# Optimization experiments

Measured on AMD Instinct MI355X. Metric: run time of the kernel, lower is better.

## Reference

```python
import jax, jax.numpy as jnp
import numpy as np

B, T, T3, P = 512, 128, 64, 12
IN1, H1 = 64, 256
IN2, H2 = 64, 256
IN3, H3 = 32, 128
GLOB, OUT = 32, 2
FC_IN = 2 * H1 + H2 + GLOB + 2 * P * H3  # 3872


def lstm_last(x, Wih, Whh, bih, bhh):
    """Single-layer batch-first LSTM (PyTorch gate order i,f,g,o); returns last hidden state [B,H]."""
    Bx = x.shape[0]
    H = Whh.shape[1]
    # precompute input projections for all timesteps: [T, B, 4H]
    xg = jnp.swapaxes(jnp.einsum('bti,gi->btg', x, Wih) + bih + bhh, 0, 1)

    def step(carry, g):
        h, c = carry
        gates = g + h @ Whh.T
        i, f, gg, o = jnp.split(gates, 4, axis=-1)
        c = jax.nn.sigmoid(f) * c + jax.nn.sigmoid(i) * jnp.tanh(gg)
        h = jax.nn.sigmoid(o) * jnp.tanh(c)
        return (h, c), None

    h0 = jnp.zeros((Bx, H), x.dtype)
    (h, _), _ = jax.lax.scan(step, (h0, h0), xg)
    return h


def setup_inputs() -> dict:
    key = jax.random.key(0)
    ks = jax.random.split(key, 20)
    n = lambda k, s: jax.random.normal(k, s, dtype=jnp.float32)
    w = lambda k, s: jax.random.normal(k, s, dtype=jnp.float32) * 0.05
    return {
        'current_game': n(ks[0], (B, GLOB)),
        'games_home': n(ks[1], (B, T, IN1)),
        'games_away': n(ks[2], (B, T, IN1)),
        'games_vs': n(ks[3], (B, T, IN2)),
        'players_home': n(ks[4], (B, P, T3, IN3)),
        'players_away': n(ks[5], (B, P, T3, IN3)),
        'Wih1': w(ks[6], (4 * H1, IN1)), 'Whh1': w(ks[7], (4 * H1, H1)),
        'bih1': w(ks[8], (4 * H1,)), 'bhh1': w(ks[9], (4 * H1,)),
        'Wih2': w(ks[10], (4 * H2, IN2)), 'Whh2': w(ks[11], (4 * H2, H2)),
        'bih2': w(ks[12], (4 * H2,)), 'bhh2': w(ks[13], (4 * H2,)),
        'Wih3': w(ks[14], (4 * H3, IN3)), 'Whh3': w(ks[15], (4 * H3, H3)),
        'bih3': w(ks[16], (4 * H3,)), 'bhh3': w(ks[17], (4 * H3,)),
        'Wfc': w(ks[18], (OUT, FC_IN)), 'bfc': w(ks[19], (OUT,)),
    }


def reference(current_game, games_home, games_away, games_vs, players_home, players_away,
              Wih1, Whh1, bih1, bhh1, Wih2, Whh2, bih2, bhh2, Wih3, Whh3, bih3, bhh3,
              Wfc, bfc):
    h_home = lstm_last(games_home, Wih1, Whh1, bih1, bhh1)   # [B, H1]
    h_away = lstm_last(games_away, Wih1, Whh1, bih1, bhh1)   # shared rnn weights
    h_vs = lstm_last(games_vs, Wih2, Whh2, bih2, bhh2)       # [B, H2]

    def players_feat(xp):
        # fold the player dim into batch: one batched LSTM pass instead of P launches
        b, p = xp.shape[0], xp.shape[1]
        h = lstm_last(xp.reshape(b * p, xp.shape[2], xp.shape[3]), Wih3, Whh3, bih3, bhh3)
        return h.reshape(b, p * H3)  # concat in player order, matching the torch loop

    feat = jnp.concatenate([
        h_home, h_away, h_vs,
        players_feat(players_home), players_feat(players_away),
        current_game,
    ], axis=1)  # [B, FC_IN]
    return feat @ Wfc.T + bfc
```

## Files before the change

### kernel.cpp

```cpp
#include <hip/hip_runtime.h>
#include <stdint.h>

typedef __bf16 bf16;
typedef bf16 bf16x8 __attribute__((ext_vector_type(8)));
typedef bf16 bf16x4 __attribute__((ext_vector_type(4)));
typedef float f32x4 __attribute__((ext_vector_type(4)));
typedef int i32x4 __attribute__((ext_vector_type(4)));

#define DEV __device__ __forceinline__

static const size_t OFF_W1 = 0;
static const size_t OFF_W2 = OFF_W1 + (size_t)640 * 1024;
static const size_t OFF_W3 = OFF_W2 + (size_t)640 * 1024;
static const size_t OFF_B1 = OFF_W3 + (size_t)160 * 1024;
static const size_t OFF_B2 = OFF_B1 + 4096;
static const size_t OFF_B3 = OFF_B2 + 4096;
static const size_t OFF_FEAT = OFF_B3 + 2048;
static const size_t WS_NEEDED = OFF_FEAT + (size_t)512 * 3840 * 4;

DEV float sigm(float x) { return 1.f / (1.f + __expf(-x)); }
DEV float tanh_(float x) { return 1.f - 2.f / (__expf(2.f * x) + 1.f); }

DEV void mfma_bv(f32x4& acc, i32x4 a, i32x4 b) {
  asm("v_mfma_f32_16x16x32_bf16 %0, %1, %2, %0" : "+a"(acc) : "v"(a), "v"(b));
}
DEV void mfma_ba(f32x4& acc, i32x4 a, i32x4 b) {
  asm("v_mfma_f32_16x16x32_bf16 %0, %1, %2, %0" : "+a"(acc) : "v"(a), "a"(b));
}

template <int H, int IN, int NT, int NKT>
DEV void packW(const float* __restrict__ Wih, const float* __restrict__ Whh,
               bf16* __restrict__ dst, int i) {
  int e = i & 7, lane = (i >> 3) & 63;
  int rest = i >> 9;
  int kt = rest % NKT; rest /= NKT;
  int nt = rest % NT;  int w = rest / NT;
  int quad = lane >> 4, l16 = lane & 15;
  constexpr int NTG = NT / 4, UW = NT * 4;
  int unit = w * UW + (nt % NTG) * 16 + l16;
  int g = nt / NTG;
  int r = g * H + unit;
  int k = kt * 32 + quad * 8 + e;
  float v = (k < IN) ? Wih[r * IN + k] : Whh[r * H + (k - IN)];
  dst[i] = (bf16)v;
}

__global__ void prep_kernel(const float* __restrict__ Wih1, const float* __restrict__ Whh1,
                            const float* __restrict__ bih1, const float* __restrict__ bhh1,
                            const float* __restrict__ Wih2, const float* __restrict__ Whh2,
                            const float* __restrict__ bih2, const float* __restrict__ bhh2,
                            const float* __restrict__ Wih3, const float* __restrict__ Whh3,
                            const float* __restrict__ bih3, const float* __restrict__ bhh3,
                            uint8_t* __restrict__ ws) {
  const int gt = blockIdx.x * blockDim.x + threadIdx.x;
  const int gs = gridDim.x * blockDim.x;
  bf16* W1 = (bf16*)(ws + OFF_W1);
  bf16* W2 = (bf16*)(ws + OFF_W2);
  bf16* W3 = (bf16*)(ws + OFF_W3);
  float* B1 = (float*)(ws + OFF_B1);
  float* B2 = (float*)(ws + OFF_B2);
  float* B3 = (float*)(ws + OFF_B3);
  for (int i = gt; i < 640 * 512; i += gs) {
    packW<256, 64, 16, 10>(Wih1, Whh1, W1, i);
    packW<256, 64, 16, 10>(Wih2, Whh2, W2, i);
  }
  for (int i = gt; i < 160 * 512; i += gs) packW<128, 32, 8, 5>(Wih3, Whh3, W3, i);
  for (int i = gt; i < 1024; i += gs) { B1[i] = bih1[i] + bhh1[i]; B2[i] = bih2[i] + bhh2[i]; }
  for (int i = gt; i < 512; i += gs) B3[i] = bih3[i] + bhh3[i];
}

template <int BM, int IN, int H, int T, int NT, int NKT, int NVV, int NVA, int NL, int NS,
          int DOM>
DEV void lstm_tile3(const float* __restrict__ x0, const float* __restrict__ x1, int halfM,
                    const bf16* __restrict__ Wd, const float* __restrict__ bsum,
                    float* __restrict__ feat, int mg, uint8_t* smem) {
  static_assert(NVV + NVA + NL + NS == NT, "split");
  static_assert((NL == 0 && NS == 0) || (NKT % 2 == 0), "wrap parity");
  constexpr int MT = BM / 16;
  constexpr int NTG = NT / 4;
  constexpr int UW = NT * 4;
  constexpr int KCH = (IN + H) / 8;
  constexpr int SROW = KCH + 1;
  constexpr int AROWE = SROW * 8;
  constexpr int XPT = BM * IN / 4 / 256;

  const int tid = threadIdx.x;
  const int lane = tid & 63;
  const int w = tid >> 6;
  const int quad = lane >> 4;
  const int l16 = lane & 15;
  const int rowbase = mg * BM;

  bf16* A = (bf16*)smem;
  bf16* Wshm = (bf16*)(smem + (size_t)BM * AROWE * 2);

  const float* xb = (rowbase < halfM) ? x0 : x1;
  const int rowoff = rowbase - ((rowbase < halfM) ? 0 : halfM);

  {
    constexpr int HCH = KCH - IN / 8;
    for (int i = tid; i < BM * HCH * 4; i += 256) {
      int row = i / (HCH * 4), rem = i % (HCH * 4);
      int chunk = IN / 8 + rem / 4, d = rem % 4;
      ((uint32_t*)A)[row * SROW * 4 + chunk * 4 + d] = 0;
    }
  }
  if constexpr (NL > 0) {
    for (int idx = tid; idx < 4 * NL * NKT * 64; idx += 256) {
      int ln = idx & 63;
      int kt = (idx >> 6) % NKT;
      int rest = (idx >> 6) / NKT;
      int nl = rest % NL, w2 = rest / NL;
      int blob = (w2 * NT + NVV + NVA + nl) * NKT + kt;
      *(bf16x8*)(Wshm + (size_t)((w2 * NL + nl) * NKT + kt) * 512 + ln * 8) =
          *(const bf16x8*)(Wd + (size_t)blob * 512 + ln * 8);
    }
  }
  i32x4 wregv[NVV > 0 ? NVV : 1][NKT];
  {
    const bf16* Wv = Wd + (size_t)(w * NT) * NKT * 512 + lane * 8;
#pragma unroll
    for (int nt = 0; nt < NVV; ++nt)
#pragma unroll
      for (int kt = 0; kt < NKT; ++kt)
        wregv[nt][kt] = *(const i32x4*)(Wv + (size_t)(nt * NKT + kt) * 512);
  }
  i32x4 wrega[NVA > 0 ? NVA : 1][NKT];
  {
    const bf16* Wa = Wd + (size_t)(w * NT + NVV) * NKT * 512 + lane * 8;
#pragma unroll
    for (int nt = 0; nt < NVA; ++nt)
#pragma unroll
      for (int kt = 0; kt < NKT; ++kt)
        wrega[nt][kt] = *(const i32x4*)(Wa + (size_t)(nt * NKT + kt) * 512);
  }
  const bf16* Wstream = Wd + (size_t)(w * NT + NVV + NVA + NL) * NKT * 512 + lane * 8;

  float bias[4][NTG];
#pragma unroll
  for (int g = 0; g < 4; ++g)
#pragma unroll
    for (int ut = 0; ut < NTG; ++ut)
      bias[g][ut] = bsum[g * H + w * UW + ut * 16 + l16];

  i32x4 sbuf[2][NS > 0 ? NS : 1];
  i32x4 wlds[2][NL > 0 ? NL : 1];

  float4 xr[XPT];
#pragma unroll
  for (int i = 0; i < XPT; ++i) {
    int idx = i * 256 + tid;
    int row = idx / (IN / 4), c4 = idx % (IN / 4);
    xr[i] = *(const float4*)(xb + (size_t)(rowoff + row) * T * IN + c4 * 4);
  }
#pragma unroll
  for (int i = 0; i < XPT; ++i) {
    int idx = i * 256 + tid;
    int row = idx / (IN / 4), c4 = idx % (IN / 4);
    int k = c4 * 4;
    bf16x4 p;
    p[0] = (bf16)xr[i].x; p[1] = (bf16)xr[i].y; p[2] = (bf16)xr[i].z; p[3] = (bf16)xr[i].w;
    *(bf16x4*)(A + row * AROWE + (k >> 3) * 8 + (k & 7)) = p;
  }
  __syncthreads();
  if constexpr (NS > 0) {
#pragma unroll
    for (int ns = 0; ns < NS; ++ns)
      sbuf[0][ns] = *(const i32x4*)(Wstream + (size_t)(ns * NKT) * 512);
  }
  if constexpr (NL > 0) {
#pragma unroll
    for (int nl = 0; nl < NL; ++nl)
      wlds[0][nl] = *(const i32x4*)(Wshm + (size_t)((w * NL + nl) * NKT) * 512 + lane * 8);
  }

  float c[MT * NTG * 4];
#pragma unroll
  for (int i = 0; i < MT * NTG * 4; ++i) c[i] = 0.f;

  f32x4 acc[NT][MT];
#pragma unroll
  for (int nt = 0; nt < NT; ++nt)
#pragma unroll
    for (int mt = 0; mt < MT; ++mt) acc[nt][mt] = f32x4{0.f, 0.f, 0.f, 0.f};

  i32x4 afbuf[2][MT];

#pragma unroll 1
  for (int t = 0; t < T; ++t) {
#pragma unroll
    for (int mt = 0; mt < MT; ++mt)
      afbuf[0][mt] = *(const i32x4*)(A + (mt * 16 + l16) * AROWE + quad * 8);
    if (t < T - 1) {
#pragma unroll
      for (int i = 0; i < XPT; ++i) {
        int idx = i * 256 + tid;
        int row = idx / (IN / 4), c4 = idx % (IN / 4);
        xr[i] =
            *(const float4*)(xb + (size_t)(rowoff + row) * T * IN + (size_t)(t + 1) * IN + c4 * 4);
      }
    }
#pragma unroll
    for (int kt = 0; kt < NKT; ++kt) {
      const int ktn = (kt + 1) % NKT;
      const int pc = kt & 1, pn = (kt + 1) & 1;
      if (kt + 1 < NKT) {
#pragma unroll
        for (int mt = 0; mt < MT; ++mt)
          afbuf[pn][mt] = *(const i32x4*)(A + (mt * 16 + l16) * AROWE + ((kt + 1) * 4 + quad) * 8);
      }
      if constexpr (NS > 0) {
#pragma unroll
        for (int ns = 0; ns < NS; ++ns)
          sbuf[pn][ns] = *(const i32x4*)(Wstream + (size_t)(ns * NKT + ktn) * 512);
      }
      if constexpr (NL > 0) {
#pragma unroll
        for (int nl = 0; nl < NL; ++nl)
          wlds[pn][nl] = *(const i32x4*)(Wshm + (size_t)((w * NL + nl) * NKT + ktn) * 512 + lane * 8);
      }
#pragma unroll
      for (int nt = 0; nt < NVV; ++nt)
#pragma unroll
        for (int mt = 0; mt < MT; ++mt) mfma_bv(acc[nt][mt], afbuf[pc][mt], wregv[nt][kt]);
#pragma unroll
      for (int nt = 0; nt < NVA; ++nt)
#pragma unroll
        for (int mt = 0; mt < MT; ++mt) mfma_ba(acc[NVV + nt][mt], afbuf[pc][mt], wrega[nt][kt]);
      if constexpr (NL > 0) {
#pragma unroll
        for (int nl = 0; nl < NL; ++nl)
#pragma unroll
          for (int mt = 0; mt < MT; ++mt)
            mfma_bv(acc[NVV + NVA + nl][mt], afbuf[pc][mt], wlds[pc][nl]);
      }
      if constexpr (NS > 0) {
#pragma unroll
        for (int ns = 0; ns < NS; ++ns)
#pragma unroll
          for (int mt = 0; mt < MT; ++mt)
            mfma_bv(acc[NVV + NVA + NL + ns][mt], afbuf[pc][mt], sbuf[pc][ns]);
      }
    }
    __syncthreads();
    asm volatile("s_nop 7\n\ts_nop 7\n\ts_nop 7" ::);

#pragma unroll
    for (int mt = 0; mt < MT; ++mt)
#pragma unroll
      for (int ut = 0; ut < NTG; ++ut)
#pragma unroll
        for (int j = 0; j < 4; ++j) {
          float gi = acc[0 * NTG + ut][mt][j] + bias[0][ut];
          float gf = acc[1 * NTG + ut][mt][j] + bias[1][ut];
          float gg = acc[2 * NTG + ut][mt][j] + bias[2][ut];
          float go = acc[3 * NTG + ut][mt][j] + bias[3][ut];
          int ci = (mt * NTG + ut) * 4 + j;
          float cc = sigm(gf) * c[ci] + sigm(gi) * tanh_(gg);
          c[ci] = cc;
          float hv = sigm(go) * tanh_(cc);
          int row = mt * 16 + quad * 4 + j;
          if (t < T - 1) {
            int k = IN + w * UW + ut * 16 + l16;
            A[row * AROWE + (k >> 3) * 8 + (k & 7)] = (bf16)hv;
          } else {
            int R = rowbase + row;
            int unit = w * UW + ut * 16 + l16;
            int b, col;
            if (DOM == 0) {
              if (R < 512) { b = R; col = unit; }
              else         { b = R - 512; col = 256 + unit; }
            } else if (DOM == 1) {
              b = R; col = 512 + unit;
            } else {
              int rr = R; int base = 768;
              if (rr >= 6144) { rr -= 6144; base = 2304; }
              b = rr / 12; int p = rr - b * 12;
              col = base + p * 128 + unit;
            }
            feat[(size_t)b * 3840 + col] = hv;
          }
        }
#pragma unroll
    for (int nt = 0; nt < NT; ++nt)
#pragma unroll
      for (int mt = 0; mt < MT; ++mt) acc[nt][mt] = f32x4{0.f, 0.f, 0.f, 0.f};
    if (t < T - 1) {
#pragma unroll
      for (int i = 0; i < XPT; ++i) {
        int idx = i * 256 + tid;
        int row = idx / (IN / 4), c4 = idx % (IN / 4);
        int k = c4 * 4;
        bf16x4 p;
        p[0] = (bf16)xr[i].x; p[1] = (bf16)xr[i].y; p[2] = (bf16)xr[i].z; p[3] = (bf16)xr[i].w;
        *(bf16x4*)(A + row * AROWE + (k >> 3) * 8 + (k & 7)) = p;
      }
    }
    __syncthreads();
  }
}

template <int NL1, int NS1>
DEV void lstm_body(const float* gh, const float* ga, const float* gv, const float* ph,
                   const float* pa, uint8_t* ws, uint8_t* smem) {
  float* feat = (float*)(ws + OFF_FEAT);
  int bid = blockIdx.x;
  if (bid < 64) {
    lstm_tile3<16, 64, 256, 128, 16, 10, 2, 4, NL1, NS1, 0>(
        gh, ga, 512, (const bf16*)(ws + OFF_W1), (const float*)(ws + OFF_B1), feat, bid, smem);
  } else if (bid < 96) {
    lstm_tile3<16, 64, 256, 128, 16, 10, 2, 4, NL1, NS1, 1>(
        gv, gv, 512, (const bf16*)(ws + OFF_W2), (const float*)(ws + OFF_B2), feat, bid - 64, smem);
  } else {
    lstm_tile3<32, 32, 128, 64, 8, 5, 8, 0, 0, 0, 2>(
        ph, pa, 6144, (const bf16*)(ws + OFF_W3), (const float*)(ws + OFF_B3), feat, bid - 96, smem);
  }
}

__global__ __launch_bounds__(256, 1) void lstm_main_big(const float* __restrict__ gh,
                                                        const float* __restrict__ ga,
                                                        const float* __restrict__ gv,
                                                        const float* __restrict__ ph,
                                                        const float* __restrict__ pa,
                                                        uint8_t* __restrict__ ws) {
  extern __shared__ uint8_t smem[];
  lstm_body<2, 8>(gh, ga, gv, ph, pa, ws, smem);
}

__global__ __launch_bounds__(256, 1) void lstm_main_small(const float* __restrict__ gh,
                                                          const float* __restrict__ ga,
                                                          const float* __restrict__ gv,
                                                          const float* __restrict__ ph,
                                                          const float* __restrict__ pa,
                                                          uint8_t* __restrict__ ws) {
  extern __shared__ uint8_t smem[];
  lstm_body<1, 9>(gh, ga, gv, ph, pa, ws, smem);
}

__global__ void fc_kernel(const float* __restrict__ feat, const float* __restrict__ cg,
                          const float* __restrict__ Wfc, const float* __restrict__ bfc,
                          float* __restrict__ out) {
  int b = blockIdx.x, tid = threadIdx.x;
  float a0 = 0.f, a1 = 0.f;
  for (int c = tid; c < 3840; c += 256) {
    float f = feat[(size_t)b * 3840 + c];
    a0 += f * Wfc[c];
    a1 += f * Wfc[3872 + c];
  }
  if (tid < 32) {
    float f = cg[b * 32 + tid];
    a0 += f * Wfc[3840 + tid];
    a1 += f * Wfc[3872 + 3840 + tid];
  }
#pragma unroll
  for (int o = 32; o > 0; o >>= 1) {
    a0 += __shfl_down(a0, o);
    a1 += __shfl_down(a1, o);
  }
  __shared__ float red[8];
  int wv = tid >> 6;
  if ((tid & 63) == 0) { red[wv * 2] = a0; red[wv * 2 + 1] = a1; }
  __syncthreads();
  if (tid == 0) {
    out[b * 2 + 0] = red[0] + red[2] + red[4] + red[6] + bfc[0];
    out[b * 2 + 1] = red[1] + red[3] + red[5] + red[7] + bfc[1];
  }
}

extern "C" void kernel_launch(void* const* d_in, const int* in_sizes, int n_in, void* d_out,
                              int out_size, void* d_ws, size_t ws_size, hipStream_t stream) {
  const float* cg = (const float*)d_in[0];
  const float* gh = (const float*)d_in[1];
  const float* ga = (const float*)d_in[2];
  const float* gv = (const float*)d_in[3];
  const float* ph = (const float*)d_in[4];
  const float* pa = (const float*)d_in[5];
  const float* Wih1 = (const float*)d_in[6];
  const float* Whh1 = (const float*)d_in[7];
  const float* bih1 = (const float*)d_in[8];
  const float* bhh1 = (const float*)d_in[9];
  const float* Wih2 = (const float*)d_in[10];
  const float* Whh2 = (const float*)d_in[11];
  const float* bih2 = (const float*)d_in[12];
  const float* bhh2 = (const float*)d_in[13];
  const float* Wih3 = (const float*)d_in[14];
  const float* Whh3 = (const float*)d_in[15];
  const float* bih3 = (const float*)d_in[16];
  const float* bhh3 = (const float*)d_in[17];
  const float* Wfc = (const float*)d_in[18];
  const float* bfc = (const float*)d_in[19];
  uint8_t* ws = (uint8_t*)d_ws;
  if (ws_size < WS_NEEDED) return;

  hipLaunchKernelGGL(prep_kernel, dim3(512), dim3(256), 0, stream, Wih1, Whh1, bih1, bhh1,
                     Wih2, Whh2, bih2, bhh2, Wih3, Whh3, bih3, bhh3, ws);

  int dev = 0, maxShm = 0;
  (void)hipGetDevice(&dev);
  (void)hipDeviceGetAttribute(&maxShm, hipDeviceAttributeMaxSharedMemoryPerBlock, dev);
  hipError_t ae = hipFuncSetAttribute((const void*)lstm_main_big,
                                      hipFuncAttributeMaxDynamicSharedMemorySize, 92416);
  if (ae == hipSuccess && maxShm >= 92416) {
    hipLaunchKernelGGL(lstm_main_big, dim3(480), dim3(256), 92416, stream, gh, ga, gv, ph, pa, ws);
  } else {
    hipLaunchKernelGGL(lstm_main_small, dim3(480), dim3(256), 51456, stream, gh, ga, gv, ph, pa,
                       ws);
  }
  hipLaunchKernelGGL(fc_kernel, dim3(512), dim3(256), 0, stream,
                     (const float*)(ws + OFF_FEAT), cg, Wfc, bfc, (float*)d_out);
}
```

Before: 1.899 ms.

## Split activations into bf16 hi/lo halves and run LSTM tiles with eight waves

```diff
diff --git a/kernel.cpp b/kernel.cpp
--- a/kernel.cpp
+++ b/kernel.cpp
@@ -24,9 +24,6 @@
 DEV void mfma_bv(f32x4& acc, i32x4 a, i32x4 b) {
   asm("v_mfma_f32_16x16x32_bf16 %0, %1, %2, %0" : "+a"(acc) : "v"(a), "v"(b));
 }
-DEV void mfma_ba(f32x4& acc, i32x4 a, i32x4 b) {
-  asm("v_mfma_f32_16x16x32_bf16 %0, %1, %2, %0" : "+a"(acc) : "v"(a), "a"(b));
-}
 
 template <int H, int IN, int NT, int NKT>
 DEV void packW(const float* __restrict__ Wih, const float* __restrict__ Whh,
@@ -36,7 +33,7 @@
   int kt = rest % NKT; rest /= NKT;
   int nt = rest % NT;  int w = rest / NT;
   int quad = lane >> 4, l16 = lane & 15;
-  constexpr int NTG = NT / 4, UW = NT * 4;
+  constexpr int NTG = NT / 4 > 0 ? NT / 4 : 1, UW = NT * 4;
   int unit = w * UW + (nt % NTG) * 16 + l16;
   int g = nt / NTG;
   int r = g * H + unit;
@@ -61,28 +58,29 @@
   float* B2 = (float*)(ws + OFF_B2);
   float* B3 = (float*)(ws + OFF_B3);
   for (int i = gt; i < 640 * 512; i += gs) {
-    packW<256, 64, 16, 10>(Wih1, Whh1, W1, i);
-    packW<256, 64, 16, 10>(Wih2, Whh2, W2, i);
-  }
-  for (int i = gt; i < 160 * 512; i += gs) packW<128, 32, 8, 5>(Wih3, Whh3, W3, i);
+    packW<256, 64, 8, 10>(Wih1, Whh1, W1, i);
+    packW<256, 64, 8, 10>(Wih2, Whh2, W2, i);
+  }
+  for (int i = gt; i < 160 * 512; i += gs) packW<128, 32, 4, 5>(Wih3, Whh3, W3, i);
   for (int i = gt; i < 1024; i += gs) { B1[i] = bih1[i] + bhh1[i]; B2[i] = bih2[i] + bhh2[i]; }
   for (int i = gt; i < 512; i += gs) B3[i] = bih3[i] + bhh3[i];
 }
 
-template <int BM, int IN, int H, int T, int NT, int NKT, int NVV, int NVA, int NL, int NS,
-          int DOM>
+template <int BM, int IN, int H, int T, int NT, int NKT, int NKTP, int NVV, int NS, int DOM>
 DEV void lstm_tile3(const float* __restrict__ x0, const float* __restrict__ x1, int halfM,
                     const bf16* __restrict__ Wd, const float* __restrict__ bsum,
                     float* __restrict__ feat, int mg, uint8_t* smem) {
-  static_assert(NVV + NVA + NL + NS == NT, "split");
-  static_assert((NL == 0 && NS == 0) || (NKT % 2 == 0), "wrap parity");
+  static_assert(NVV + NS == NT, "split");
+  static_assert(NKT == 2 * NKTP, "hi/lo split layout");
+  static_assert(NS == 0 || (NKT % 2 == 0), "wrap parity");
   constexpr int MT = BM / 16;
-  constexpr int NTG = NT / 4;
+  constexpr int NTG = NT / 4 > 0 ? NT / 4 : 1;
   constexpr int UW = NT * 4;
-  constexpr int KCH = (IN + H) / 8;
-  constexpr int SROW = KCH + 1;
+  constexpr int HALFK = NKTP * 32;
+  constexpr int SROW = NKT * 4 + 1;
   constexpr int AROWE = SROW * 8;
-  constexpr int XPT = BM * IN / 4 / 256;
+  constexpr int XQ = BM * IN / 4;
+  constexpr int XPT = (XQ + 511) / 512;
 
   const int tid = threadIdx.x;
   const int lane = tid & 63;
@@ -92,49 +90,23 @@
   const int rowbase = mg * BM;
 
   bf16* A = (bf16*)smem;
-  bf16* Wshm = (bf16*)(smem + (size_t)BM * AROWE * 2);
 
   const float* xb = (rowbase < halfM) ? x0 : x1;
   const int rowoff = rowbase - ((rowbase < halfM) ? 0 : halfM);
 
+  for (int i = tid; i < BM * AROWE / 2; i += 512) ((uint32_t*)A)[i] = 0;
+  __syncthreads();
+
+  i32x4 wregv[NVV > 0 ? NVV : 1][NKTP];
   {
-    constexpr int HCH = KCH - IN / 8;
-    for (int i = tid; i < BM * HCH * 4; i += 256) {
-      int row = i / (HCH * 4), rem = i % (HCH * 4);
-      int chunk = IN / 8 + rem / 4, d = rem % 4;
-      ((uint32_t*)A)[row * SROW * 4 + chunk * 4 + d] = 0;
-    }
-  }
-  if constexpr (NL > 0) {
-    for (int idx = tid; idx < 4 * NL * NKT * 64; idx += 256) {
-      int ln = idx & 63;
-      int kt = (idx >> 6) % NKT;
-      int rest = (idx >> 6) / NKT;
-      int nl = rest % NL, w2 = rest / NL;
-      int blob = (w2 * NT + NVV + NVA + nl) * NKT + kt;
-      *(bf16x8*)(Wshm + (size_t)((w2 * NL + nl) * NKT + kt) * 512 + ln * 8) =
-          *(const bf16x8*)(Wd + (size_t)blob * 512 + ln * 8);
-    }
-  }
-  i32x4 wregv[NVV > 0 ? NVV : 1][NKT];
-  {
-    const bf16* Wv = Wd + (size_t)(w * NT) * NKT * 512 + lane * 8;
+    const bf16* Wv = Wd + (size_t)(w * NT) * NKTP * 512 + lane * 8;
 #pragma unroll
     for (int nt = 0; nt < NVV; ++nt)
 #pragma unroll
-      for (int kt = 0; kt < NKT; ++kt)
-        wregv[nt][kt] = *(const i32x4*)(Wv + (size_t)(nt * NKT + kt) * 512);
-  }
-  i32x4 wrega[NVA > 0 ? NVA : 1][NKT];
-  {
-    const bf16* Wa = Wd + (size_t)(w * NT + NVV) * NKT * 512 + lane * 8;
-#pragma unroll
-    for (int nt = 0; nt < NVA; ++nt)
-#pragma unroll
-      for (int kt = 0; kt < NKT; ++kt)
-        wrega[nt][kt] = *(const i32x4*)(Wa + (size_t)(nt * NKT + kt) * 512);
-  }
-  const bf16* Wstream = Wd + (size_t)(w * NT + NVV + NVA + NL) * NKT * 512 + lane * 8;
+      for (int kt = 0; kt < NKTP; ++kt)
+        wregv[nt][kt] = *(const i32x4*)(Wv + (size_t)(nt * NKTP + kt) * 512);
+  }
+  const bf16* Wstream = Wd + (size_t)(w * NT + NVV) * NKTP * 512 + lane * 8;
 
   float bias[4][NTG];
 #pragma unroll
@@ -144,34 +116,37 @@
       bias[g][ut] = bsum[g * H + w * UW + ut * 16 + l16];
 
   i32x4 sbuf[2][NS > 0 ? NS : 1];
-  i32x4 wlds[2][NL > 0 ? NL : 1];
 
   float4 xr[XPT];
 #pragma unroll
   for (int i = 0; i < XPT; ++i) {
-    int idx = i * 256 + tid;
-    int row = idx / (IN / 4), c4 = idx % (IN / 4);
-    xr[i] = *(const float4*)(xb + (size_t)(rowoff + row) * T * IN + c4 * 4);
+    int idx = i * 512 + tid;
+    if (idx < XQ) {
+      int row = idx / (IN / 4), c4 = idx % (IN / 4);
+      xr[i] = *(const float4*)(xb + (size_t)(rowoff + row) * T * IN + c4 * 4);
+    }
   }
 #pragma unroll
   for (int i = 0; i < XPT; ++i) {
-    int idx = i * 256 + tid;
-    int row = idx / (IN / 4), c4 = idx % (IN / 4);
-    int k = c4 * 4;
-    bf16x4 p;
-    p[0] = (bf16)xr[i].x; p[1] = (bf16)xr[i].y; p[2] = (bf16)xr[i].z; p[3] = (bf16)xr[i].w;
-    *(bf16x4*)(A + row * AROWE + (k >> 3) * 8 + (k & 7)) = p;
+    int idx = i * 512 + tid;
+    if (idx < XQ) {
+      int row = idx / (IN / 4), c4 = idx % (IN / 4);
+      int k = c4 * 4;
+      bf16x4 p, q;
+      p[0] = (bf16)xr[i].x; q[0] = (bf16)(xr[i].x - (float)p[0]);
+      p[1] = (bf16)xr[i].y; q[1] = (bf16)(xr[i].y - (float)p[1]);
+      p[2] = (bf16)xr[i].z; q[2] = (bf16)(xr[i].z - (float)p[2]);
+      p[3] = (bf16)xr[i].w; q[3] = (bf16)(xr[i].w - (float)p[3]);
+      *(bf16x4*)(A + row * AROWE + (k >> 3) * 8 + (k & 7)) = p;
+      int kl = k + HALFK;
+      *(bf16x4*)(A + row * AROWE + (kl >> 3) * 8 + (kl & 7)) = q;
+    }
   }
   __syncthreads();
   if constexpr (NS > 0) {
 #pragma unroll
     for (int ns = 0; ns < NS; ++ns)
-      sbuf[0][ns] = *(const i32x4*)(Wstream + (size_t)(ns * NKT) * 512);
-  }
-  if constexpr (NL > 0) {
-#pragma unroll
-    for (int nl = 0; nl < NL; ++nl)
-      wlds[0][nl] = *(const i32x4*)(Wshm + (size_t)((w * NL + nl) * NKT) * 512 + lane * 8);
+      sbuf[0][ns] = *(const i32x4*)(Wstream + (size_t)(ns * NKTP) * 512);
   }
 
   float c[MT * NTG * 4];
@@ -194,15 +169,19 @@
     if (t < T - 1) {
 #pragma unroll
       for (int i = 0; i < XPT; ++i) {
-        int idx = i * 256 + tid;
-        int row = idx / (IN / 4), c4 = idx % (IN / 4);
-        xr[i] =
-            *(const float4*)(xb + (size_t)(rowoff + row) * T * IN + (size_t)(t + 1) * IN + c4 * 4);
+        int idx = i * 512 + tid;
+        if (idx < XQ) {
+          int row = idx / (IN / 4), c4 = idx % (IN / 4);
+          xr[i] = *(const float4*)(xb + (size_t)(rowoff + row) * T * IN +
+                                   (size_t)(t + 1) * IN + c4 * 4);
+        }
       }
     }
 #pragma unroll
     for (int kt = 0; kt < NKT; ++kt) {
+      const int ktp = (kt < NKTP) ? kt : kt - NKTP;
       const int ktn = (kt + 1) % NKT;
+      const int ktpn = (ktn < NKTP) ? ktn : ktn - NKTP;
       const int pc = kt & 1, pn = (kt + 1) & 1;
       if (kt + 1 < NKT) {
 #pragma unroll
@@ -212,34 +191,18 @@
       if constexpr (NS > 0) {
 #pragma unroll
         for (int ns = 0; ns < NS; ++ns)
-          sbuf[pn][ns] = *(const i32x4*)(Wstream + (size_t)(ns * NKT + ktn) * 512);
-      }
-      if constexpr (NL > 0) {
-#pragma unroll
-        for (int nl = 0; nl < NL; ++nl)
-          wlds[pn][nl] = *(const i32x4*)(Wshm + (size_t)((w * NL + nl) * NKT + ktn) * 512 + lane * 8);
+          sbuf[pn][ns] = *(const i32x4*)(Wstream + (size_t)(ns * NKTP + ktpn) * 512);
       }
 #pragma unroll
       for (int nt = 0; nt < NVV; ++nt)
 #pragma unroll
-        for (int mt = 0; mt < MT; ++mt) mfma_bv(acc[nt][mt], afbuf[pc][mt], wregv[nt][kt]);
-#pragma unroll
-      for (int nt = 0; nt < NVA; ++nt)
-#pragma unroll
-        for (int mt = 0; mt < MT; ++mt) mfma_ba(acc[NVV + nt][mt], afbuf[pc][mt], wrega[nt][kt]);
-      if constexpr (NL > 0) {
-#pragma unroll
-        for (int nl = 0; nl < NL; ++nl)
+        for (int mt = 0; mt < MT; ++mt) mfma_bv(acc[nt][mt], afbuf[pc][mt], wregv[nt][ktp]);
+      if constexpr (NS > 0) {
+#pragma unroll
+        for (int ns = 0; ns < NS; ++ns)
 #pragma unroll
           for (int mt = 0; mt < MT; ++mt)
-            mfma_bv(acc[NVV + NVA + nl][mt], afbuf[pc][mt], wlds[pc][nl]);
-      }
-      if constexpr (NS > 0) {
-#pragma unroll
-        for (int ns = 0; ns < NS; ++ns)
-#pragma unroll
-          for (int mt = 0; mt < MT; ++mt)
-            mfma_bv(acc[NVV + NVA + NL + ns][mt], afbuf[pc][mt], sbuf[pc][ns]);
+            mfma_bv(acc[NVV + ns][mt], afbuf[pc][mt], sbuf[pc][ns]);
       }
     }
     __syncthreads();
@@ -261,8 +224,11 @@
           float hv = sigm(go) * tanh_(cc);
           int row = mt * 16 + quad * 4 + j;
           if (t < T - 1) {
-            int k = IN + w * UW + ut * 16 + l16;
-            A[row * AROWE + (k >> 3) * 8 + (k & 7)] = (bf16)hv;
+            int kg = IN + w * UW + ut * 16 + l16;
+            bf16 hb = (bf16)hv;
+            A[row * AROWE + (kg >> 3) * 8 + (kg & 7)] = hb;
+            int kl = kg + HALFK;
+            A[row * AROWE + (kl >> 3) * 8 + (kl & 7)] = (bf16)(hv - (float)hb);
           } else {
             int R = rowbase + row;
             int unit = w * UW + ut * 16 + l16;
@@ -288,53 +254,44 @@
     if (t < T - 1) {
 #pragma unroll
       for (int i = 0; i < XPT; ++i) {
-        int idx = i * 256 + tid;
-        int row = idx / (IN / 4), c4 = idx % (IN / 4);
-        int k = c4 * 4;
-        bf16x4 p;
-        p[0] = (bf16)xr[i].x; p[1] = (bf16)xr[i].y; p[2] = (bf16)xr[i].z; p[3] = (bf16)xr[i].w;
-        *(bf16x4*)(A + row * AROWE + (k >> 3) * 8 + (k & 7)) = p;
+        int idx = i * 512 + tid;
+        if (idx < XQ) {
+          int row = idx / (IN / 4), c4 = idx % (IN / 4);
+          int k = c4 * 4;
+          bf16x4 p, q;
+          p[0] = (bf16)xr[i].x; q[0] = (bf16)(xr[i].x - (float)p[0]);
+          p[1] = (bf16)xr[i].y; q[1] = (bf16)(xr[i].y - (float)p[1]);
+          p[2] = (bf16)xr[i].z; q[2] = (bf16)(xr[i].z - (float)p[2]);
+          p[3] = (bf16)xr[i].w; q[3] = (bf16)(xr[i].w - (float)p[3]);
+          *(bf16x4*)(A + row * AROWE + (k >> 3) * 8 + (k & 7)) = p;
+          int kl = k + HALFK;
+          *(bf16x4*)(A + row * AROWE + (kl >> 3) * 8 + (kl & 7)) = q;
+        }
       }
     }
     __syncthreads();
   }
 }
 
-template <int NL1, int NS1>
-DEV void lstm_body(const float* gh, const float* ga, const float* gv, const float* ph,
-                   const float* pa, uint8_t* ws, uint8_t* smem) {
+__global__ __launch_bounds__(512, 2) void lstm_main(const float* __restrict__ gh,
+                                                    const float* __restrict__ ga,
+                                                    const float* __restrict__ gv,
+                                                    const float* __restrict__ ph,
+                                                    const float* __restrict__ pa,
+                                                    uint8_t* __restrict__ ws) {
+  extern __shared__ uint8_t smem[];
   float* feat = (float*)(ws + OFF_FEAT);
   int bid = blockIdx.x;
   if (bid < 64) {
-    lstm_tile3<16, 64, 256, 128, 16, 10, 2, 4, NL1, NS1, 0>(
+    lstm_tile3<16, 64, 256, 128, 8, 20, 10, 2, 6, 0>(
         gh, ga, 512, (const bf16*)(ws + OFF_W1), (const float*)(ws + OFF_B1), feat, bid, smem);
   } else if (bid < 96) {
-    lstm_tile3<16, 64, 256, 128, 16, 10, 2, 4, NL1, NS1, 1>(
+    lstm_tile3<16, 64, 256, 128, 8, 20, 10, 2, 6, 1>(
         gv, gv, 512, (const bf16*)(ws + OFF_W2), (const float*)(ws + OFF_B2), feat, bid - 64, smem);
   } else {
-    lstm_tile3<32, 32, 128, 64, 8, 5, 8, 0, 0, 0, 2>(
+    lstm_tile3<32, 32, 128, 64, 4, 10, 5, 4, 0, 2>(
         ph, pa, 6144, (const bf16*)(ws + OFF_W3), (const float*)(ws + OFF_B3), feat, bid - 96, smem);
   }
-}
-
-__global__ __launch_bounds__(256, 1) void lstm_main_big(const float* __restrict__ gh,
-                                                        const float* __restrict__ ga,
-                                                        const float* __restrict__ gv,
-                                                        const float* __restrict__ ph,
-                                                        const float* __restrict__ pa,
-                                                        uint8_t* __restrict__ ws) {
-  extern __shared__ uint8_t smem[];
-  lstm_body<2, 8>(gh, ga, gv, ph, pa, ws, smem);
-}
-
-__global__ __launch_bounds__(256, 1) void lstm_main_small(const float* __restrict__ gh,
-                                                          const float* __restrict__ ga,
-                                                          const float* __restrict__ gv,
-                                                          const float* __restrict__ ph,
-                                                          const float* __restrict__ pa,
-                                                          uint8_t* __restrict__ ws) {
-  extern __shared__ uint8_t smem[];
-  lstm_body<1, 9>(gh, ga, gv, ph, pa, ws, smem);
 }
 
 __global__ void fc_kernel(const float* __restrict__ feat, const float* __restrict__ cg,
@@ -395,17 +352,8 @@
   hipLaunchKernelGGL(prep_kernel, dim3(512), dim3(256), 0, stream, Wih1, Whh1, bih1, bhh1,
                      Wih2, Whh2, bih2, bhh2, Wih3, Whh3, bih3, bhh3, ws);
 
-  int dev = 0, maxShm = 0;
-  (void)hipGetDevice(&dev);
-  (void)hipDeviceGetAttribute(&maxShm, hipDeviceAttributeMaxSharedMemoryPerBlock, dev);
-  hipError_t ae = hipFuncSetAttribute((const void*)lstm_main_big,
-                                      hipFuncAttributeMaxDynamicSharedMemorySize, 92416);
-  if (ae == hipSuccess && maxShm >= 92416) {
-    hipLaunchKernelGGL(lstm_main_big, dim3(480), dim3(256), 92416, stream, gh, ga, gv, ph, pa, ws);
-  } else {
-    hipLaunchKernelGGL(lstm_main_small, dim3(480), dim3(256), 51456, stream, gh, ga, gv, ph, pa,
-                       ws);
-  }
+  hipLaunchKernelGGL(lstm_main, dim3(480), dim3(512), 20992, stream, gh, ga, gv, ph, pa, ws);
+
   hipLaunchKernelGGL(fc_kernel, dim3(512), dim3(256), 0, stream,
                      (const float*)(ws + OFF_FEAT), cg, Wfc, bfc, (float*)d_out);
 }
```

Result: slower. 6.542 ms (+244.4%).
